# Kernel optimization log

Measured on AMD Instinct MI355X. Metric: run time of the kernel, lower is better.

The kernel has to match this reference:

```python
import jax, jax.numpy as jnp
import numpy as np

B, D, E, H, L = 32768, 512, 10, 128, 2  # batch, input_dim, max_charts, expert hidden, latent_dim
RH1, RH2 = 256, 128                      # router hidden sizes
TAU = 3.0


def setup_inputs() -> dict:
    key = jax.random.key(0)
    ks = jax.random.split(key, 16)
    rnd = lambda k, *s: (jax.random.normal(k, s, jnp.float32) * 0.05)
    return {
        "x": jax.random.normal(ks[0], (B, D), jnp.float32),
        "u": jax.random.uniform(ks[1], (B, E), jnp.float32),
        # router params (last layer init ~ N(0, 0.01), bias 0, as in _init_router)
        "rw1": rnd(ks[2], D, RH1), "rb1": jnp.zeros((RH1,), jnp.float32),
        "rw2": rnd(ks[3], RH1, RH2), "rb2": jnp.zeros((RH2,), jnp.float32),
        "rw3": jax.random.normal(ks[4], (RH2, E), jnp.float32) * 0.01,
        "rb3": jnp.zeros((E,), jnp.float32),
        # stacked expert params: all 10 experts batched along leading dim
        "ew1": rnd(ks[5], E, D, H), "eb1": rnd(ks[6], E, H),
        "ew2": rnd(ks[7], E, H, H), "eb2": rnd(ks[8], E, H),
        "ew3": rnd(ks[9], E, H, L), "eb3": rnd(ks[10], E, L),
    }


def reference(x, u, rw1, rb1, rw2, rb2, rw3, rb3, ew1, eb1, ew2, eb2, ew3, eb3):
    # router MLP: D -> 256 -> 128 -> E
    h = jax.nn.relu(x @ rw1 + rb1)
    h = jax.nn.relu(h @ rw2 + rb2)
    logits = h @ rw3 + rb3                                  # [B, E]
    # gumbel_softmax(tau=3.0, hard=False): softmax((logits + gumbel)/tau)
    g = -jnp.log(-jnp.log(jnp.clip(u, 1e-10, 1.0)) + 1e-10)
    weights = jax.nn.softmax((logits + g) / TAU, axis=1)    # [B, E]
    # all 10 experts as batched GEMMs (fuses the python loop over charts)
    h1 = jax.nn.relu(jnp.einsum('bi,eio->beo', x, ew1) + eb1[None])   # [B, E, H]
    h2 = jax.nn.relu(jnp.einsum('beh,eho->beo', h1, ew2) + eb2[None]) # [B, E, H]
    zc = jnp.einsum('beh,ehl->bel', h2, ew3) + eb3[None]              # [B, E, L]
    z = jnp.einsum('be,bel->bl', weights, zc)                         # [B, L]
    chart_outputs = jnp.transpose(zc, (1, 0, 2))                      # [E, B, L]
    return z, weights, chart_outputs
```

## Files before the change

### kernel.cpp

```cpp
#include <hip/hip_runtime.h>
#include <stdint.h>

typedef __bf16 bf16x8 __attribute__((ext_vector_type(8)));
typedef float floatx4 __attribute__((ext_vector_type(4)));
typedef unsigned short ushort_t;

__device__ __forceinline__ ushort_t bf16rne(float f) {
    union { float f; unsigned u; } v; v.f = f;
    return (ushort_t)((v.u + 0x7fffu + ((v.u >> 16) & 1u)) >> 16);
}

__device__ __forceinline__ void gl_lds16(const ushort_t* g, ushort_t* l) {
    __builtin_amdgcn_global_load_lds(
        (const __attribute__((address_space(1))) unsigned int*)g,
        (__attribute__((address_space(3))) unsigned int*)l, 16, 0, 0);
}


__device__ __forceinline__ void transpose_body(const float* __restrict__ in,
                                               ushort_t* __restrict__ outp,
                                               int idx, int K, int N, int total) {
    if (idx >= total) return;
    int kn = K * N;
    int e = idx / kn;
    int r = idx - e * kn;
    int n = r / K;
    int k = r - n * K;
    outp[idx] = bf16rne(in[e * kn + k * N + n]);
}

__global__ void prep(const float* __restrict__ x, ushort_t* __restrict__ x16,
                     const float* __restrict__ ew1, ushort_t* __restrict__ ew1t,
                     const float* __restrict__ ew2, ushort_t* __restrict__ ew2t,
                     const float* __restrict__ rw1, ushort_t* __restrict__ rw1t,
                     const float* __restrict__ rw2, ushort_t* __restrict__ rw2t) {
    int b = blockIdx.x, tid = threadIdx.x;
    if (b < 16384) {
        int i = b * 256 + tid;
        float4 f = ((const float4*)x)[i];
        union { ushort_t s[4]; uint2 v; } pk;
        pk.s[0] = bf16rne(f.x); pk.s[1] = bf16rne(f.y);
        pk.s[2] = bf16rne(f.z); pk.s[3] = bf16rne(f.w);
        ((uint2*)x16)[i] = pk.v;
    } else if (b < 18944) {
        transpose_body(ew1, ew1t, (b - 16384) * 256 + tid, 512, 128, 655360);
    } else if (b < 19584) {
        transpose_body(ew2, ew2t, (b - 18944) * 256 + tid, 128, 128, 163840);
    } else if (b < 20096) {
        transpose_body(rw1, rw1t, (b - 19584) * 256 + tid, 512, 256, 131072);
    } else {
        transpose_body(rw2, rw2t, (b - 20096) * 256 + tid, 256, 128, 32768);
    }
}

__global__ __launch_bounds__(256, 4)
void router_l1(const ushort_t* __restrict__ x16, const ushort_t* __restrict__ rw1t,
               const float* __restrict__ rb1, ushort_t* __restrict__ hr1) {
    __shared__ alignas(16) ushort_t sXW[8192];
    __shared__ float sBias[128];

    const int tid = threadIdx.x;
    const int rb = blockIdx.x, nb = blockIdx.y;
    const int wave = tid >> 6, lane = tid & 63;
    const int ln15 = lane & 15, q = lane >> 4;
    const int wm = (wave & 1) * 64, wn = (wave >> 1) * 64;
    const int mhalf = wm >> 6, nhalf = wn >> 6;

    if (tid < 128) sBias[tid] = rb1[nb * 128 + tid];

    const ushort_t* xblk = x16 + (size_t)rb * 128 * 512;
    const ushort_t* wbase = rw1t + (size_t)nb * 128 * 512;

    const int rl = lane >> 2, cl = lane & 3;
    const int sw = (cl ^ ((rl >> 1) & 3)) * 8;
    const int rg0 = wave * 2, rg1 = wave * 2 + 1;
    const int fslot = (4 * ln15 + (q ^ ((ln15 >> 1) & 3))) * 8;

    floatx4 acc[4][4];
#pragma unroll
    for (int i = 0; i < 4; ++i)
#pragma unroll
        for (int j = 0; j < 4; ++j) acc[i][j] = (floatx4){0.f, 0.f, 0.f, 0.f};

    for (int k0 = 0; k0 < 512; k0 += 32) {
        __syncthreads();
        gl_lds16(xblk + (size_t)(rg0 * 16 + rl) * 512 + k0 + sw, &sXW[rg0 * 512]);
        gl_lds16(xblk + (size_t)(rg1 * 16 + rl) * 512 + k0 + sw, &sXW[rg1 * 512]);
        gl_lds16(wbase + (size_t)(rg0 * 16 + rl) * 512 + k0 + sw, &sXW[4096 + rg0 * 512]);
        gl_lds16(wbase + (size_t)(rg1 * 16 + rl) * 512 + k0 + sw, &sXW[4096 + rg1 * 512]);
        __syncthreads();
        bf16x8 a[4], b[4];
#pragma unroll
        for (int t = 0; t < 4; ++t) a[t] = *(const bf16x8*)(&sXW[4096 + (mhalf * 4 + t) * 512 + fslot]);
#pragma unroll
        for (int t = 0; t < 4; ++t) b[t] = *(const bf16x8*)(&sXW[(nhalf * 4 + t) * 512 + fslot]);
#pragma unroll
        for (int i = 0; i < 4; ++i)
#pragma unroll
            for (int j = 0; j < 4; ++j)
                acc[i][j] = __builtin_amdgcn_mfma_f32_16x16x32_bf16(a[i], b[j], acc[i][j], 0, 0, 0);
    }

    const int rbase = rb * 128;
#pragma unroll
    for (int i = 0; i < 4; ++i) {
        int n0 = wm + i * 16 + q * 4;
#pragma unroll
        for (int j = 0; j < 4; ++j) {
            int row = wn + j * 16 + ln15;
            union { ushort_t s[4]; uint2 v; } pk;
#pragma unroll
            for (int r = 0; r < 4; ++r)
                pk.s[r] = bf16rne(fmaxf(acc[i][j][r] + sBias[n0 + r], 0.f));
            *(uint2*)(&hr1[(size_t)(rbase + row) * 256 + nb * 128 + n0]) = pk.v;
        }
    }
}

__global__ __launch_bounds__(256, 2)
void router2(const ushort_t* __restrict__ hr1, const ushort_t* __restrict__ rw2t,
             const float* __restrict__ rb2, const float* __restrict__ rw3,
             const float* __restrict__ rb3, const float* __restrict__ u,
             float* __restrict__ wts, float* __restrict__ z) {
    __shared__ alignas(16) ushort_t sXW[8192];
    __shared__ float sw3[1280];
    __shared__ float sBias[128];
    __shared__ float lgbuf[128][10];

    const int tid = threadIdx.x;
    const int rb = blockIdx.x;
    const int wave = tid >> 6, lane = tid & 63;
    const int ln15 = lane & 15, q = lane >> 4;
    const int wm = (wave & 1) * 64, wn = (wave >> 1) * 64;
    const int mhalf = wm >> 6, nhalf = wn >> 6;

    for (int i = tid; i < 1280; i += 256) sw3[i] = rw3[i];
    if (tid < 128) sBias[tid] = rb2[tid];

    const ushort_t* brow = hr1 + (size_t)rb * 128 * 256;
    const int rl = lane >> 2, cl = lane & 3;
    const int sw = (cl ^ ((rl >> 1) & 3)) * 8;
    const int rg0 = wave * 2, rg1 = wave * 2 + 1;
    const int fslot = (4 * ln15 + (q ^ ((ln15 >> 1) & 3))) * 8;

    floatx4 acc2[4][4];
#pragma unroll
    for (int i = 0; i < 4; ++i)
#pragma unroll
        for (int j = 0; j < 4; ++j) acc2[i][j] = (floatx4){0.f, 0.f, 0.f, 0.f};

    for (int k0 = 0; k0 < 256; k0 += 32) {
        __syncthreads();
        gl_lds16(brow + (size_t)(rg0 * 16 + rl) * 256 + k0 + sw, &sXW[rg0 * 512]);
        gl_lds16(brow + (size_t)(rg1 * 16 + rl) * 256 + k0 + sw, &sXW[rg1 * 512]);
        gl_lds16(rw2t + (size_t)(rg0 * 16 + rl) * 256 + k0 + sw, &sXW[4096 + rg0 * 512]);
        gl_lds16(rw2t + (size_t)(rg1 * 16 + rl) * 256 + k0 + sw, &sXW[4096 + rg1 * 512]);
        __syncthreads();
        bf16x8 a[4], b[4];
#pragma unroll
        for (int t = 0; t < 4; ++t) a[t] = *(const bf16x8*)(&sXW[4096 + (mhalf * 4 + t) * 512 + fslot]);
#pragma unroll
        for (int t = 0; t < 4; ++t) b[t] = *(const bf16x8*)(&sXW[(nhalf * 4 + t) * 512 + fslot]);
#pragma unroll
        for (int i = 0; i < 4; ++i)
#pragma unroll
            for (int j = 0; j < 4; ++j)
                acc2[i][j] = __builtin_amdgcn_mfma_f32_16x16x32_bf16(a[i], b[j], acc2[i][j], 0, 0, 0);
    }

    float lg[4][10];
#pragma unroll
    for (int j = 0; j < 4; ++j)
#pragma unroll
        for (int ee = 0; ee < 10; ++ee) lg[j][ee] = 0.f;
#pragma unroll
    for (int i = 0; i < 4; ++i) {
#pragma unroll
        for (int r = 0; r < 4; ++r) {
            int n = wm + i * 16 + q * 4 + r;
            float bias = sBias[n];
            const float* w3r = &sw3[n * 10];
#pragma unroll
            for (int j = 0; j < 4; ++j) {
                float val = fmaxf(acc2[i][j][r] + bias, 0.f);
#pragma unroll
                for (int ee = 0; ee < 10; ++ee) lg[j][ee] += val * w3r[ee];
            }
        }
    }
#pragma unroll
    for (int j = 0; j < 4; ++j)
#pragma unroll
        for (int ee = 0; ee < 10; ++ee) {
            lg[j][ee] += __shfl_xor(lg[j][ee], 16, 64);
            lg[j][ee] += __shfl_xor(lg[j][ee], 32, 64);
        }
    if (wm == 0 && q == 0) {
#pragma unroll
        for (int j = 0; j < 4; ++j) {
            int row = wn + 16 * j + ln15;
#pragma unroll
            for (int ee = 0; ee < 10; ++ee) lgbuf[row][ee] = lg[j][ee];
        }
    }
    __syncthreads();
    if (wm == 64 && q == 0) {
#pragma unroll
        for (int j = 0; j < 4; ++j) {
            int row = wn + 16 * j + ln15;
#pragma unroll
            for (int ee = 0; ee < 10; ++ee) lgbuf[row][ee] += lg[j][ee];
        }
    }
    __syncthreads();
    if (tid < 128) {
        int grow = rb * 128 + tid;
        float v[10], mx = -1e30f;
#pragma unroll
        for (int ee = 0; ee < 10; ++ee) {
            float uu = u[(size_t)grow * 10 + ee];
            uu = fminf(fmaxf(uu, 1e-10f), 1.0f);
            float g = -logf(-logf(uu) + 1e-10f);
            v[ee] = (lgbuf[tid][ee] + rb3[ee] + g) * (1.0f / 3.0f);
            mx = fmaxf(mx, v[ee]);
        }
        float s = 0.f;
#pragma unroll
        for (int ee = 0; ee < 10; ++ee) { v[ee] = expf(v[ee] - mx); s += v[ee]; }
        float inv = 1.0f / s;
#pragma unroll
        for (int ee = 0; ee < 10; ++ee) wts[(size_t)grow * 10 + ee] = v[ee] * inv;
    }
    z[rb * 256 + tid] = 0.f;
}

__global__ __launch_bounds__(256, 3)
void expert_fused(const ushort_t* __restrict__ x16, const ushort_t* __restrict__ ew1t,
                  const ushort_t* __restrict__ ew2t, const float* __restrict__ eb1,
                  const float* __restrict__ eb2, const float* __restrict__ ew3,
                  const float* __restrict__ eb3, const float* __restrict__ wts,
                  float* __restrict__ chart, float* __restrict__ z) {
    __shared__ alignas(16) ushort_t sXW[8192];
    __shared__ alignas(16) ushort_t sH1[16384];
    __shared__ float sB1[128];
    __shared__ float sB2[128];
    __shared__ float sW3[256];
    __shared__ float zbuf[128][2];

    const int tid = threadIdx.x;
    const int id = blockIdx.x;
    const int xcd = id & 7, local = id >> 3;
    const int e = local % 10;
    const int rb = xcd * 32 + local / 10;

    const int wave = tid >> 6, lane = tid & 63;
    const int ln15 = lane & 15, q = lane >> 4;
    const int wm = (wave & 1) * 64, wn = (wave >> 1) * 64;
    const int mhalf = wm >> 6, nhalf = wn >> 6;

    if (tid < 128) sB1[tid] = eb1[e * 128 + tid];
    else sB2[tid - 128] = eb2[e * 128 + (tid - 128)];
    sW3[tid] = ew3[e * 256 + tid];

    const ushort_t* xblk = x16 + (size_t)rb * 128 * 512;
    const ushort_t* w1 = ew1t + (size_t)e * 128 * 512;
    const ushort_t* w2 = ew2t + (size_t)e * 128 * 128;

    const int rl = lane >> 2, cl = lane & 3;
    const int sw = (cl ^ ((rl >> 1) & 3)) * 8;
    const int rg0 = wave * 2, rg1 = wave * 2 + 1;
    const int fslot = (4 * ln15 + (q ^ ((ln15 >> 1) & 3))) * 8;

    {
        floatx4 acc[4][4];
#pragma unroll
        for (int i = 0; i < 4; ++i)
#pragma unroll
            for (int j = 0; j < 4; ++j) acc[i][j] = (floatx4){0.f, 0.f, 0.f, 0.f};

        for (int k0 = 0; k0 < 512; k0 += 32) {
            __syncthreads();
            gl_lds16(xblk + (size_t)(rg0 * 16 + rl) * 512 + k0 + sw, &sXW[rg0 * 512]);
            gl_lds16(xblk + (size_t)(rg1 * 16 + rl) * 512 + k0 + sw, &sXW[rg1 * 512]);
            gl_lds16(w1 + (size_t)(rg0 * 16 + rl) * 512 + k0 + sw, &sXW[4096 + rg0 * 512]);
            gl_lds16(w1 + (size_t)(rg1 * 16 + rl) * 512 + k0 + sw, &sXW[4096 + rg1 * 512]);
            __syncthreads();
            bf16x8 a[4], b[4];
#pragma unroll
            for (int t = 0; t < 4; ++t) a[t] = *(const bf16x8*)(&sXW[4096 + (mhalf * 4 + t) * 512 + fslot]);
#pragma unroll
            for (int t = 0; t < 4; ++t) b[t] = *(const bf16x8*)(&sXW[(nhalf * 4 + t) * 512 + fslot]);
#pragma unroll
            for (int i = 0; i < 4; ++i)
#pragma unroll
                for (int j = 0; j < 4; ++j)
                    acc[i][j] = __builtin_amdgcn_mfma_f32_16x16x32_bf16(a[i], b[j], acc[i][j], 0, 0, 0);
        }

#pragma unroll
        for (int i = 0; i < 4; ++i) {
            int hbase = wm + 16 * i;
            int kh = hbase >> 5;
            int qhi = (hbase >> 4) & 1;
            int slotq = 2 * qhi + (q >> 1);
            int h0 = hbase + q * 4;
#pragma unroll
            for (int j = 0; j < 4; ++j) {
                union { ushort_t s[4]; uint2 v; } pk;
#pragma unroll
                for (int r = 0; r < 4; ++r)
                    pk.s[r] = bf16rne(fmaxf(acc[i][j][r] + sB1[h0 + r], 0.f));
                *(uint2*)(&sH1[kh * 4096 + (nhalf * 4 + j) * 512 + slotq * 128 + ln15 * 8 + (q & 1) * 4]) = pk.v;
            }
        }
    }

    floatx4 acc2[4][4];
#pragma unroll
    for (int i = 0; i < 4; ++i)
#pragma unroll
        for (int j = 0; j < 4; ++j) acc2[i][j] = (floatx4){0.f, 0.f, 0.f, 0.f};

    for (int p = 0; p < 2; ++p) {
        __syncthreads();
#pragma unroll
        for (int r = 0; r < 4; ++r) {
            int s = wave * 4 + r;
            int khl = s >> 3, rg = s & 7;
            int kh = p * 2 + khl;
            gl_lds16(w2 + (size_t)(rg * 16 + rl) * 128 + kh * 32 + sw, &sXW[s * 512]);
        }
        __syncthreads();
#pragma unroll
        for (int khl = 0; khl < 2; ++khl) {
            int kh = p * 2 + khl;
            bf16x8 a[4], b[4];
#pragma unroll
            for (int t = 0; t < 4; ++t) a[t] = *(const bf16x8*)(&sXW[(khl * 8 + mhalf * 4 + t) * 512 + fslot]);
#pragma unroll
            for (int t = 0; t < 4; ++t) b[t] = *(const bf16x8*)(&sH1[kh * 4096 + (nhalf * 4 + t) * 512 + lane * 8]);
#pragma unroll
            for (int i = 0; i < 4; ++i)
#pragma unroll
                for (int j = 0; j < 4; ++j)
                    acc2[i][j] = __builtin_amdgcn_mfma_f32_16x16x32_bf16(a[i], b[j], acc2[i][j], 0, 0, 0);
        }
    }

    float zc0[4] = {0.f, 0.f, 0.f, 0.f}, zc1[4] = {0.f, 0.f, 0.f, 0.f};
#pragma unroll
    for (int i = 0; i < 4; ++i) {
        int o0 = wm + i * 16 + q * 4;
#pragma unroll
        for (int r = 0; r < 4; ++r) {
            int o = o0 + r;
            float w3a = sW3[2 * o], w3b = sW3[2 * o + 1];
            float bias = sB2[o];
#pragma unroll
            for (int j = 0; j < 4; ++j) {
                float val = fmaxf(acc2[i][j][r] + bias, 0.f);
                zc0[j] += val * w3a;
                zc1[j] += val * w3b;
            }
        }
    }
#pragma unroll
    for (int j = 0; j < 4; ++j) {
        zc0[j] += __shfl_xor(zc0[j], 16, 64);
        zc0[j] += __shfl_xor(zc0[j], 32, 64);
        zc1[j] += __shfl_xor(zc1[j], 16, 64);
        zc1[j] += __shfl_xor(zc1[j], 32, 64);
    }
    if (wm == 0 && q == 0) {
#pragma unroll
        for (int j = 0; j < 4; ++j) {
            int row = wn + j * 16 + ln15;
            zbuf[row][0] = zc0[j];
            zbuf[row][1] = zc1[j];
        }
    }
    __syncthreads();
    if (wm == 64 && q == 0) {
#pragma unroll
        for (int j = 0; j < 4; ++j) {
            int row = wn + j * 16 + ln15;
            zbuf[row][0] += zc0[j];
            zbuf[row][1] += zc1[j];
        }
    }
    __syncthreads();
    {
        int row = tid >> 1, l = tid & 1;
        int grow = rb * 128 + row;
        float vz = zbuf[row][l] + eb3[e * 2 + l];
        chart[(size_t)e * 65536 + (size_t)grow * 2 + l] = vz;
        atomicAdd(&z[(size_t)grow * 2 + l], wts[(size_t)grow * 10 + e] * vz);
    }
}

extern "C" void kernel_launch(void* const* d_in, const int* in_sizes, int n_in,
                              void* d_out, int out_size, void* d_ws, size_t ws_size,
                              hipStream_t stream) {
    const float* x = (const float*)d_in[0];
    const float* u = (const float*)d_in[1];
    const float* rw1 = (const float*)d_in[2];
    const float* rb1 = (const float*)d_in[3];
    const float* rw2 = (const float*)d_in[4];
    const float* rb2 = (const float*)d_in[5];
    const float* rw3 = (const float*)d_in[6];
    const float* rb3 = (const float*)d_in[7];
    const float* ew1 = (const float*)d_in[8];
    const float* eb1 = (const float*)d_in[9];
    const float* ew2 = (const float*)d_in[10];
    const float* eb2 = (const float*)d_in[11];
    const float* ew3 = (const float*)d_in[12];
    const float* eb3 = (const float*)d_in[13];
    float* out = (float*)d_out;
    float* z = out;
    float* wts = out + 65536;
    float* chart = out + 393216;

    ushort_t* x16  = (ushort_t*)d_ws;
    ushort_t* ew1t = x16 + 16777216;
    ushort_t* ew2t = ew1t + 655360;
    ushort_t* rw1t = ew2t + 163840;
    ushort_t* rw2t = rw1t + 131072;
    ushort_t* hr1  = rw2t + 32768;

    prep<<<20224, 256, 0, stream>>>(x, x16, ew1, ew1t, ew2, ew2t, rw1, rw1t, rw2, rw2t);

    router_l1<<<dim3(256, 2), 256, 0, stream>>>(x16, rw1t, rb1, hr1);
    router2<<<256, 256, 0, stream>>>(hr1, rw2t, rb2, rw3, rb3, u, wts, z);

    expert_fused<<<2560, 256, 0, stream>>>(x16, ew1t, ew2t, eb1, eb2, ew3, eb3,
                                           wts, chart, z);
}
```

Baseline: 224.6 us.

## Load weight MFMA fragments directly from global and tile the weight transpose

The router and expert GEMMs now read the weight (A) operand fragments straight from global memory into registers instead of staging them through LDS. This halves the LDS tile, so occupancy can rise, and it removes the staged W2 loads and two barriers in the expert second layer. The prep kernel's elementwise weight transpose is replaced by a 64x64 LDS-tiled transpose so both reads and writes are coalesced, which also reduces the prep grid. In exchange, weight reads become per-wave global loads that rely on cache hits, and the MFMAs may stall on global latency because there is no prefetch.

```diff
diff --git a/kernel.cpp b/kernel.cpp
--- a/kernel.cpp
+++ b/kernel.cpp
@@ -16,24 +16,13 @@
         (__attribute__((address_space(3))) unsigned int*)l, 16, 0, 0);
 }
 
-
-__device__ __forceinline__ void transpose_body(const float* __restrict__ in,
-                                               ushort_t* __restrict__ outp,
-                                               int idx, int K, int N, int total) {
-    if (idx >= total) return;
-    int kn = K * N;
-    int e = idx / kn;
-    int r = idx - e * kn;
-    int n = r / K;
-    int k = r - n * K;
-    outp[idx] = bf16rne(in[e * kn + k * N + n]);
-}
 
 __global__ void prep(const float* __restrict__ x, ushort_t* __restrict__ x16,
                      const float* __restrict__ ew1, ushort_t* __restrict__ ew1t,
                      const float* __restrict__ ew2, ushort_t* __restrict__ ew2t,
                      const float* __restrict__ rw1, ushort_t* __restrict__ rw1t,
                      const float* __restrict__ rw2, ushort_t* __restrict__ rw2t) {
+    __shared__ ushort_t sT[64 * 65];
     int b = blockIdx.x, tid = threadIdx.x;
     if (b < 16384) {
         int i = b * 256 + tid;
@@ -42,21 +31,46 @@
         pk.s[0] = bf16rne(f.x); pk.s[1] = bf16rne(f.y);
         pk.s[2] = bf16rne(f.z); pk.s[3] = bf16rne(f.w);
         ((uint2*)x16)[i] = pk.v;
-    } else if (b < 18944) {
-        transpose_body(ew1, ew1t, (b - 16384) * 256 + tid, 512, 128, 655360);
-    } else if (b < 19584) {
-        transpose_body(ew2, ew2t, (b - 18944) * 256 + tid, 128, 128, 163840);
-    } else if (b < 20096) {
-        transpose_body(rw1, rw1t, (b - 19584) * 256 + tid, 512, 256, 131072);
+        return;
+    }
+    const float* in; ushort_t* outp; int K, N, k0, n0;
+    int i = b - 16384;
+    if (i < 160) {
+        int e = i >> 4, t = i & 15;
+        in = ew1 + e * 65536; outp = ew1t + e * 65536;
+        K = 512; N = 128; k0 = (t >> 1) * 64; n0 = (t & 1) * 64;
+    } else if (i < 200) {
+        i -= 160; int e = i >> 2, t = i & 3;
+        in = ew2 + e * 16384; outp = ew2t + e * 16384;
+        K = 128; N = 128; k0 = (t >> 1) * 64; n0 = (t & 1) * 64;
+    } else if (i < 232) {
+        i -= 200; in = rw1; outp = rw1t;
+        K = 512; N = 256; k0 = (i >> 2) * 64; n0 = (i & 3) * 64;
     } else {
-        transpose_body(rw2, rw2t, (b - 20096) * 256 + tid, 256, 128, 32768);
+        i -= 232; in = rw2; outp = rw2t;
+        K = 256; N = 128; k0 = (i >> 1) * 64; n0 = (i & 1) * 64;
+    }
+    {
+        int c = tid & 63, r0 = tid >> 6;
+#pragma unroll
+        for (int p = 0; p < 16; ++p) {
+            int r = r0 * 16 + p;
+            sT[c * 65 + r] = bf16rne(in[(size_t)(k0 + r) * N + n0 + c]);
+        }
+        __syncthreads();
+        int rr = tid & 63, c0 = tid >> 6;
+#pragma unroll
+        for (int p = 0; p < 16; ++p) {
+            int cc = c0 * 16 + p;
+            outp[(size_t)(n0 + cc) * K + k0 + rr] = sT[cc * 65 + rr];
+        }
     }
 }
 
 __global__ __launch_bounds__(256, 4)
 void router_l1(const ushort_t* __restrict__ x16, const ushort_t* __restrict__ rw1t,
                const float* __restrict__ rb1, ushort_t* __restrict__ hr1) {
-    __shared__ alignas(16) ushort_t sXW[8192];
+    __shared__ alignas(16) ushort_t sX[4096];
     __shared__ float sBias[128];
 
     const int tid = threadIdx.x;
@@ -64,16 +78,16 @@
     const int wave = tid >> 6, lane = tid & 63;
     const int ln15 = lane & 15, q = lane >> 4;
     const int wm = (wave & 1) * 64, wn = (wave >> 1) * 64;
-    const int mhalf = wm >> 6, nhalf = wn >> 6;
+    const int nhalf = wn >> 6;
 
     if (tid < 128) sBias[tid] = rb1[nb * 128 + tid];
 
     const ushort_t* xblk = x16 + (size_t)rb * 128 * 512;
-    const ushort_t* wbase = rw1t + (size_t)nb * 128 * 512;
+    const ushort_t* wrow = rw1t + (size_t)(nb * 128 + wm + ln15) * 512 + q * 8;
 
     const int rl = lane >> 2, cl = lane & 3;
     const int sw = (cl ^ ((rl >> 1) & 3)) * 8;
-    const int rg0 = wave * 2, rg1 = wave * 2 + 1;
+    const int rg0 = wave * 2, rg1 = rg0 + 1;
     const int fslot = (4 * ln15 + (q ^ ((ln15 >> 1) & 3))) * 8;
 
     floatx4 acc[4][4];
@@ -84,16 +98,14 @@
 
     for (int k0 = 0; k0 < 512; k0 += 32) {
         __syncthreads();
-        gl_lds16(xblk + (size_t)(rg0 * 16 + rl) * 512 + k0 + sw, &sXW[rg0 * 512]);
-        gl_lds16(xblk + (size_t)(rg1 * 16 + rl) * 512 + k0 + sw, &sXW[rg1 * 512]);
-        gl_lds16(wbase + (size_t)(rg0 * 16 + rl) * 512 + k0 + sw, &sXW[4096 + rg0 * 512]);
-        gl_lds16(wbase + (size_t)(rg1 * 16 + rl) * 512 + k0 + sw, &sXW[4096 + rg1 * 512]);
+        gl_lds16(xblk + (size_t)(rg0 * 16 + rl) * 512 + k0 + sw, &sX[rg0 * 512]);
+        gl_lds16(xblk + (size_t)(rg1 * 16 + rl) * 512 + k0 + sw, &sX[rg1 * 512]);
         __syncthreads();
         bf16x8 a[4], b[4];
 #pragma unroll
-        for (int t = 0; t < 4; ++t) a[t] = *(const bf16x8*)(&sXW[4096 + (mhalf * 4 + t) * 512 + fslot]);
-#pragma unroll
-        for (int t = 0; t < 4; ++t) b[t] = *(const bf16x8*)(&sXW[(nhalf * 4 + t) * 512 + fslot]);
+        for (int t = 0; t < 4; ++t) a[t] = *(const bf16x8*)(wrow + (size_t)t * 16 * 512 + k0);
+#pragma unroll
+        for (int t = 0; t < 4; ++t) b[t] = *(const bf16x8*)(&sX[(nhalf * 4 + t) * 512 + fslot]);
 #pragma unroll
         for (int i = 0; i < 4; ++i)
 #pragma unroll
@@ -122,7 +134,7 @@
              const float* __restrict__ rb2, const float* __restrict__ rw3,
              const float* __restrict__ rb3, const float* __restrict__ u,
              float* __restrict__ wts, float* __restrict__ z) {
-    __shared__ alignas(16) ushort_t sXW[8192];
+    __shared__ alignas(16) ushort_t sB[4096];
     __shared__ float sw3[1280];
     __shared__ float sBias[128];
     __shared__ float lgbuf[128][10];
@@ -132,15 +144,16 @@
     const int wave = tid >> 6, lane = tid & 63;
     const int ln15 = lane & 15, q = lane >> 4;
     const int wm = (wave & 1) * 64, wn = (wave >> 1) * 64;
-    const int mhalf = wm >> 6, nhalf = wn >> 6;
+    const int nhalf = wn >> 6;
 
     for (int i = tid; i < 1280; i += 256) sw3[i] = rw3[i];
     if (tid < 128) sBias[tid] = rb2[tid];
 
     const ushort_t* brow = hr1 + (size_t)rb * 128 * 256;
+    const ushort_t* arow = rw2t + (size_t)(wm + ln15) * 256 + q * 8;
     const int rl = lane >> 2, cl = lane & 3;
     const int sw = (cl ^ ((rl >> 1) & 3)) * 8;
-    const int rg0 = wave * 2, rg1 = wave * 2 + 1;
+    const int rg0 = wave * 2, rg1 = rg0 + 1;
     const int fslot = (4 * ln15 + (q ^ ((ln15 >> 1) & 3))) * 8;
 
     floatx4 acc2[4][4];
@@ -151,16 +164,14 @@
 
     for (int k0 = 0; k0 < 256; k0 += 32) {
         __syncthreads();
-        gl_lds16(brow + (size_t)(rg0 * 16 + rl) * 256 + k0 + sw, &sXW[rg0 * 512]);
-        gl_lds16(brow + (size_t)(rg1 * 16 + rl) * 256 + k0 + sw, &sXW[rg1 * 512]);
-        gl_lds16(rw2t + (size_t)(rg0 * 16 + rl) * 256 + k0 + sw, &sXW[4096 + rg0 * 512]);
-        gl_lds16(rw2t + (size_t)(rg1 * 16 + rl) * 256 + k0 + sw, &sXW[4096 + rg1 * 512]);
+        gl_lds16(brow + (size_t)(rg0 * 16 + rl) * 256 + k0 + sw, &sB[rg0 * 512]);
+        gl_lds16(brow + (size_t)(rg1 * 16 + rl) * 256 + k0 + sw, &sB[rg1 * 512]);
         __syncthreads();
         bf16x8 a[4], b[4];
 #pragma unroll
-        for (int t = 0; t < 4; ++t) a[t] = *(const bf16x8*)(&sXW[4096 + (mhalf * 4 + t) * 512 + fslot]);
-#pragma unroll
-        for (int t = 0; t < 4; ++t) b[t] = *(const bf16x8*)(&sXW[(nhalf * 4 + t) * 512 + fslot]);
+        for (int t = 0; t < 4; ++t) a[t] = *(const bf16x8*)(arow + (size_t)t * 16 * 256 + k0);
+#pragma unroll
+        for (int t = 0; t < 4; ++t) b[t] = *(const bf16x8*)(&sB[(nhalf * 4 + t) * 512 + fslot]);
 #pragma unroll
         for (int i = 0; i < 4; ++i)
 #pragma unroll
@@ -240,7 +251,7 @@
                   const float* __restrict__ eb2, const float* __restrict__ ew3,
                   const float* __restrict__ eb3, const float* __restrict__ wts,
                   float* __restrict__ chart, float* __restrict__ z) {
-    __shared__ alignas(16) ushort_t sXW[8192];
+    __shared__ alignas(16) ushort_t sX[4096];
     __shared__ alignas(16) ushort_t sH1[16384];
     __shared__ float sB1[128];
     __shared__ float sB2[128];
@@ -256,19 +267,19 @@
     const int wave = tid >> 6, lane = tid & 63;
     const int ln15 = lane & 15, q = lane >> 4;
     const int wm = (wave & 1) * 64, wn = (wave >> 1) * 64;
-    const int mhalf = wm >> 6, nhalf = wn >> 6;
+    const int nhalf = wn >> 6;
 
     if (tid < 128) sB1[tid] = eb1[e * 128 + tid];
     else sB2[tid - 128] = eb2[e * 128 + (tid - 128)];
     sW3[tid] = ew3[e * 256 + tid];
 
     const ushort_t* xblk = x16 + (size_t)rb * 128 * 512;
-    const ushort_t* w1 = ew1t + (size_t)e * 128 * 512;
-    const ushort_t* w2 = ew2t + (size_t)e * 128 * 128;
+    const ushort_t* w1row = ew1t + (size_t)e * 128 * 512 + (size_t)(wm + ln15) * 512 + q * 8;
+    const ushort_t* w2row = ew2t + (size_t)e * 128 * 128 + (size_t)(wm + ln15) * 128 + q * 8;
 
     const int rl = lane >> 2, cl = lane & 3;
     const int sw = (cl ^ ((rl >> 1) & 3)) * 8;
-    const int rg0 = wave * 2, rg1 = wave * 2 + 1;
+    const int rg0 = wave * 2, rg1 = rg0 + 1;
     const int fslot = (4 * ln15 + (q ^ ((ln15 >> 1) & 3))) * 8;
 
     {
@@ -280,16 +291,14 @@
 
         for (int k0 = 0; k0 < 512; k0 += 32) {
             __syncthreads();
-            gl_lds16(xblk + (size_t)(rg0 * 16 + rl) * 512 + k0 + sw, &sXW[rg0 * 512]);
-            gl_lds16(xblk + (size_t)(rg1 * 16 + rl) * 512 + k0 + sw, &sXW[rg1 * 512]);
-            gl_lds16(w1 + (size_t)(rg0 * 16 + rl) * 512 + k0 + sw, &sXW[4096 + rg0 * 512]);
-            gl_lds16(w1 + (size_t)(rg1 * 16 + rl) * 512 + k0 + sw, &sXW[4096 + rg1 * 512]);
+            gl_lds16(xblk + (size_t)(rg0 * 16 + rl) * 512 + k0 + sw, &sX[rg0 * 512]);
+            gl_lds16(xblk + (size_t)(rg1 * 16 + rl) * 512 + k0 + sw, &sX[rg1 * 512]);
             __syncthreads();
             bf16x8 a[4], b[4];
 #pragma unroll
-            for (int t = 0; t < 4; ++t) a[t] = *(const bf16x8*)(&sXW[4096 + (mhalf * 4 + t) * 512 + fslot]);
-#pragma unroll
-            for (int t = 0; t < 4; ++t) b[t] = *(const bf16x8*)(&sXW[(nhalf * 4 + t) * 512 + fslot]);
+            for (int t = 0; t < 4; ++t) a[t] = *(const bf16x8*)(w1row + (size_t)t * 16 * 512 + k0);
+#pragma unroll
+            for (int t = 0; t < 4; ++t) b[t] = *(const bf16x8*)(&sX[(nhalf * 4 + t) * 512 + fslot]);
 #pragma unroll
             for (int i = 0; i < 4; ++i)
 #pragma unroll
@@ -321,30 +330,19 @@
 #pragma unroll
         for (int j = 0; j < 4; ++j) acc2[i][j] = (floatx4){0.f, 0.f, 0.f, 0.f};
 
-    for (int p = 0; p < 2; ++p) {
-        __syncthreads();
-#pragma unroll
-        for (int r = 0; r < 4; ++r) {
-            int s = wave * 4 + r;
-            int khl = s >> 3, rg = s & 7;
-            int kh = p * 2 + khl;
-            gl_lds16(w2 + (size_t)(rg * 16 + rl) * 128 + kh * 32 + sw, &sXW[s * 512]);
-        }
-        __syncthreads();
-#pragma unroll
-        for (int khl = 0; khl < 2; ++khl) {
-            int kh = p * 2 + khl;
-            bf16x8 a[4], b[4];
-#pragma unroll
-            for (int t = 0; t < 4; ++t) a[t] = *(const bf16x8*)(&sXW[(khl * 8 + mhalf * 4 + t) * 512 + fslot]);
-#pragma unroll
-            for (int t = 0; t < 4; ++t) b[t] = *(const bf16x8*)(&sH1[kh * 4096 + (nhalf * 4 + t) * 512 + lane * 8]);
-#pragma unroll
-            for (int i = 0; i < 4; ++i)
-#pragma unroll
-                for (int j = 0; j < 4; ++j)
-                    acc2[i][j] = __builtin_amdgcn_mfma_f32_16x16x32_bf16(a[i], b[j], acc2[i][j], 0, 0, 0);
-        }
+    __syncthreads();
+#pragma unroll
+    for (int kh = 0; kh < 4; ++kh) {
+        bf16x8 a[4], b[4];
+#pragma unroll
+        for (int t = 0; t < 4; ++t) a[t] = *(const bf16x8*)(w2row + (size_t)t * 16 * 128 + kh * 32);
+#pragma unroll
+        for (int t = 0; t < 4; ++t) b[t] = *(const bf16x8*)(&sH1[kh * 4096 + (nhalf * 4 + t) * 512 + lane * 8]);
+#pragma unroll
+        for (int i = 0; i < 4; ++i)
+#pragma unroll
+            for (int j = 0; j < 4; ++j)
+                acc2[i][j] = __builtin_amdgcn_mfma_f32_16x16x32_bf16(a[i], b[j], acc2[i][j], 0, 0, 0);
     }
 
     float zc0[4] = {0.f, 0.f, 0.f, 0.f}, zc1[4] = {0.f, 0.f, 0.f, 0.f};
@@ -427,7 +425,7 @@
     ushort_t* rw2t = rw1t + 131072;
     ushort_t* hr1  = rw2t + 32768;
 
-    prep<<<20224, 256, 0, stream>>>(x, x16, ew1, ew1t, ew2, ew2t, rw1, rw1t, rw2, rw2t);
+    prep<<<16624, 256, 0, stream>>>(x, x16, ew1, ew1t, ew2, ew2t, rw1, rw1t, rw2, rw2t);
 
     router_l1<<<dim3(256, 2), 256, 0, stream>>>(x16, rw1t, rb1, hr1);
     router2<<<256, 256, 0, stream>>>(hr1, rw2t, rb2, rw3, rb3, u, wts, z);
```

Result: slower. 287.5 us (+28.0%).
